# Kernel optimization log

Measured on AMD Instinct MI355X. Metric: run time of the kernel, lower is better.

## Reference

```python
import jax, jax.numpy as jnp
import numpy as np

B, T, H = 16, 512, 512

def _gru_layer(x, h0, wih, whh, bih, bhh, reverse):
    # x: [B,T,in], h0: [B,H]; PyTorch gate order r,z,n in the 3H axis.
    xg = jnp.einsum('bti,gi->btg', x, wih) + bih  # [B,T,3H] input-side gates, precomputed
    def step(h, xg_t):
        gh = h @ whh.T + bhh  # [B,3H]
        xr, xz, xn = jnp.split(xg_t, 3, axis=-1)
        hr, hz, hn = jnp.split(gh, 3, axis=-1)
        r = jax.nn.sigmoid(xr + hr)
        z = jax.nn.sigmoid(xz + hz)
        n = jnp.tanh(xn + r * hn)
        h_new = (1.0 - z) * n + z * h
        return h_new, h_new
    _, ys = jax.lax.scan(step, h0, jnp.swapaxes(xg, 0, 1), reverse=reverse)  # [T,B,H]
    return jnp.swapaxes(ys, 0, 1)

def _forward(x, h1, h2,
             wih_l0f, whh_l0f, bih_l0f, bhh_l0f, wih_l0b, whh_l0b, bih_l0b, bhh_l0b,
             wih_l1f, whh_l1f, bih_l1f, bhh_l1f, wih_l1b, whh_l1b, bih_l1b, bhh_l1b,
             wih_l2f, whh_l2f, bih_l2f, bhh_l2f, wih_l2b, whh_l2b, bih_l2b, bhh_l2b,
             g2_wih, g2_whh, g2_bih, g2_bhh, fc_w, fc_b):
    layers = [((wih_l0f, whh_l0f, bih_l0f, bhh_l0f), (wih_l0b, whh_l0b, bih_l0b, bhh_l0b)),
              ((wih_l1f, whh_l1f, bih_l1f, bhh_l1f), (wih_l1b, whh_l1b, bih_l1b, bhh_l1b)),
              ((wih_l2f, whh_l2f, bih_l2f, bhh_l2f), (wih_l2b, whh_l2b, bih_l2b, bhh_l2b))]
    out = x
    for l, (pf, pb) in enumerate(layers):
        of = _gru_layer(out, h1[2 * l], *pf, reverse=False)
        ob = _gru_layer(out, h1[2 * l + 1], *pb, reverse=True)
        out = jnp.concatenate([of, ob], axis=-1)  # [B,T,2H]
    out2 = _gru_layer(out, h2[0], g2_wih, g2_whh, g2_bih, g2_bhh, reverse=False)  # [B,T,H]
    logits = out2[:, -1, :] @ fc_w.T + fc_b  # [B,1]
    return (jax.nn.sigmoid(logits), out2)

def setup_inputs():
    key = jax.random.key(0)
    ks = jax.random.split(key, 40)
    cnt = iter(range(40))
    s = jnp.float32(0.04)
    d = {}
    d['x'] = jax.random.normal(ks[next(cnt)], (B, T, 2048), jnp.float32)
    d['h1'] = jax.random.normal(ks[next(cnt)], (6, B, H), jnp.float32) * s
    d['h2'] = jax.random.normal(ks[next(cnt)], (1, B, H), jnp.float32) * s
    in_dims = [2048, 2 * H, 2 * H]
    for l in range(3):
        for dr in 'fb':
            d[f'wih_l{l}{dr}'] = jax.random.normal(ks[next(cnt)], (3 * H, in_dims[l]), jnp.float32) * s
            d[f'whh_l{l}{dr}'] = jax.random.normal(ks[next(cnt)], (3 * H, H), jnp.float32) * s
            d[f'bih_l{l}{dr}'] = jax.random.normal(ks[next(cnt)], (3 * H,), jnp.float32) * s
            d[f'bhh_l{l}{dr}'] = jax.random.normal(ks[next(cnt)], (3 * H,), jnp.float32) * s
    d['g2_wih'] = jax.random.normal(ks[next(cnt)], (3 * H, 2 * H), jnp.float32) * s
    d['g2_whh'] = jax.random.normal(ks[next(cnt)], (3 * H, H), jnp.float32) * s
    d['g2_bih'] = jax.random.normal(ks[next(cnt)], (3 * H,), jnp.float32) * s
    d['g2_bhh'] = jax.random.normal(ks[next(cnt)], (3 * H,), jnp.float32) * s
    d['fc_w'] = jax.random.normal(ks[next(cnt)], (1, H), jnp.float32) * s
    d['fc_b'] = jax.random.normal(ks[next(cnt)], (1,), jnp.float32) * s
    return d

def reference(x, h1, h2,
              wih_l0f, whh_l0f, bih_l0f, bhh_l0f, wih_l0b, whh_l0b, bih_l0b, bhh_l0b,
              wih_l1f, whh_l1f, bih_l1f, bhh_l1f, wih_l1b, whh_l1b, bih_l1b, bhh_l1b,
              wih_l2f, whh_l2f, bih_l2f, bhh_l2f, wih_l2b, whh_l2b, bih_l2b, bhh_l2b,
              g2_wih, g2_whh, g2_bih, g2_bhh, fc_w, fc_b):
    return _forward(x, h1, h2,
                    wih_l0f, whh_l0f, bih_l0f, bhh_l0f, wih_l0b, whh_l0b, bih_l0b, bhh_l0b,
                    wih_l1f, whh_l1f, bih_l1f, bhh_l1f, wih_l1b, whh_l1b, bih_l1b, bhh_l1b,
                    wih_l2f, whh_l2f, bih_l2f, bhh_l2f, wih_l2b, whh_l2b, bih_l2b, bhh_l2b,
                    g2_wih, g2_whh, g2_bih, g2_bhh, fc_w, fc_b)
```

## Files before the change

### kernel.cpp

```cpp
#include <hip/hip_runtime.h>
#include <cstdint>
#include <cstddef>

typedef unsigned short u16;
typedef unsigned int u32;
typedef __attribute__((ext_vector_type(8))) short bf16x8;
typedef __attribute__((ext_vector_type(4))) float f32x4;

#define T_SEQ 512
#define HID 512

__device__ __forceinline__ u16 f2bf(float f) {
  union { float f; u32 i; } c; c.f = f;
  u32 r = (c.i + 0x7FFFu + ((c.i >> 16) & 1u)) >> 16;
  return (u16)r;
}
__device__ __forceinline__ u16 f2h(float f) {
  union { _Float16 h; u16 u; } c; c.h = (_Float16)f; return c.u;
}
__device__ __forceinline__ float h2f(u16 u) {
  union { u16 u; _Float16 h; } c; c.u = u; return (float)c.h;
}
__device__ __forceinline__ float sigmf(float x) { return 1.f / (1.f + __expf(-x)); }
__device__ __forceinline__ float tanhfast(float x) {
  float e = __expf(2.f * x); return 1.f - 2.f / (e + 1.f);
}

template <int AF32>
__launch_bounds__(256)
__global__ void gemm_xg(const void* __restrict__ Av,
                        const float* __restrict__ W0, const float* __restrict__ W1,
                        const float* __restrict__ b0, const float* __restrict__ b1,
                        u16* __restrict__ xg0, u16* __restrict__ xg1, int K) {
  const int dir = blockIdx.z;
  const float* W = dir ? W1 : W0;
  const float* bias = dir ? b1 : b0;
  u16* xg = dir ? xg1 : xg0;
  const int bm = blockIdx.x, bn = blockIdx.y;
  const int tid = threadIdx.x, lane = tid & 63, wv = tid >> 6;
  const int wm = wv & 1, wn = wv >> 1, quad = lane >> 4, l15 = lane & 15;

  __shared__ u16 As[128 * 40];
  __shared__ u16 Bs[128 * 40];

  f32x4 acc[4][4] = {};
  const float* Wb = W + (size_t)(bn * 128) * K;

  for (int k0 = 0; k0 < K; k0 += 32) {
    __syncthreads();
    if constexpr (AF32) {
      const float* Ab = (const float*)Av + (size_t)(bm * 128) * K;
#pragma unroll
      for (int it = 0; it < 4; ++it) {
        int c = tid + it * 256;
        int row = c >> 3, kp = (c & 7) * 4;
        float4 v = *(const float4*)(Ab + (size_t)row * K + k0 + kp);
        ushort4 s = { f2bf(v.x), f2bf(v.y), f2bf(v.z), f2bf(v.w) };
        *(ushort4*)(&As[row * 40 + kp]) = s;
      }
    } else {
      const u16* Ab = (const u16*)Av + (size_t)(bm * 128) * K;
#pragma unroll
      for (int it = 0; it < 2; ++it) {
        int c = tid + it * 256;
        int row = c >> 2, kp = (c & 3) * 8;
        *(bf16x8*)(&As[row * 40 + kp]) = *(const bf16x8*)(Ab + (size_t)row * K + k0 + kp);
      }
    }
#pragma unroll
    for (int it = 0; it < 4; ++it) {
      int c = tid + it * 256;
      int row = c >> 3, kp = (c & 7) * 4;
      float4 v = *(const float4*)(Wb + (size_t)row * K + k0 + kp);
      ushort4 s = { f2bf(v.x), f2bf(v.y), f2bf(v.z), f2bf(v.w) };
      *(ushort4*)(&Bs[row * 40 + kp]) = s;
    }
    __syncthreads();
    bf16x8 af[4], bf[4];
#pragma unroll
    for (int i = 0; i < 4; ++i) {
      af[i] = *(const bf16x8*)(&As[(wm * 64 + i * 16 + l15) * 40 + quad * 8]);
      bf[i] = *(const bf16x8*)(&Bs[(wn * 64 + i * 16 + l15) * 40 + quad * 8]);
    }
#pragma unroll
    for (int mi = 0; mi < 4; ++mi)
#pragma unroll
      for (int ni = 0; ni < 4; ++ni)
        acc[mi][ni] = __builtin_amdgcn_mfma_f32_16x16x32_bf16(af[mi], bf[ni], acc[mi][ni], 0, 0, 0);
  }

#pragma unroll
  for (int ni = 0; ni < 4; ++ni) {
    int n = bn * 128 + wn * 64 + ni * 16 + l15;
    float bv = bias[n];
#pragma unroll
    for (int mi = 0; mi < 4; ++mi) {
      int m0 = bm * 128 + wm * 64 + mi * 16 + quad * 4;
#pragma unroll
      for (int r = 0; r < 4; ++r)
        xg[(size_t)(m0 + r) * 1536 + n] = f2h(acc[mi][ni][r] + bv);
    }
  }
}

__launch_bounds__(384, 1)
__global__ void gru_rec(const u16* __restrict__ xg_f, const u16* __restrict__ xg_b,
                        const float* __restrict__ whh_f, const float* __restrict__ whh_b,
                        const float* __restrict__ bhh_f, const float* __restrict__ bhh_b,
                        const float* __restrict__ h0_f, const float* __restrict__ h0_b,
                        void* __restrict__ outp, int out_stride, int out_f32,
                        u16* __restrict__ hbuf, int* __restrict__ counters, int Tn) {
  const int dir = blockIdx.y;
  const u16* xg   = dir ? xg_b  : xg_f;
  const float* whh = dir ? whh_b : whh_f;
  const float* bhh = dir ? bhh_b : bhh_f;
  const float* h0  = dir ? h0_b  : h0_f;
  const int w = blockIdx.x;
  const int tid = threadIdx.x, lane = tid & 63, wv = tid >> 6;
  const int quad = lane >> 4, l15 = lane & 15;
  int* cnt = counters + dir * 1024;
  u16* hb0 = hbuf + (dir * 2 + 0) * (16 * 512);
  u16* hb1 = hbuf + (dir * 2 + 1) * (16 * 512);
  const int dir_off = dir * 512;

  __shared__ float glds[3][16][64];
  __shared__ float hprev[16][64];
  __shared__ u16 xlds[3][16][64];
  __shared__ float bhl[3][64];

  bf16x8 bfr[2][16];
#pragma unroll
  for (int f = 0; f < 2; ++f) {
    int fl = wv * 2 + f;
    int g = fl >> 2, q = fl & 3;
    int row = g * 512 + (w * 4 + q) * 16 + l15;
    const float* wp = whh + (size_t)row * 512 + quad * 8;
#pragma unroll
    for (int kt = 0; kt < 16; ++kt) {
      float4 a = *(const float4*)(wp + kt * 32);
      float4 b = *(const float4*)(wp + kt * 32 + 4);
      bf16x8 fr;
      fr[0] = (short)f2bf(a.x); fr[1] = (short)f2bf(a.y);
      fr[2] = (short)f2bf(a.z); fr[3] = (short)f2bf(a.w);
      fr[4] = (short)f2bf(b.x); fr[5] = (short)f2bf(b.y);
      fr[6] = (short)f2bf(b.z); fr[7] = (short)f2bf(b.w);
      bfr[f][kt] = fr;
    }
  }
  for (int i = tid; i < 512; i += 384) {
    int b = i >> 5, j2 = (i & 31) * 2;
    float v0 = h0[b * 512 + w * 64 + j2];
    float v1 = h0[b * 512 + w * 64 + j2 + 1];
    hprev[b][j2] = v0; hprev[b][j2 + 1] = v1;
    u32 pk = (u32)f2bf(v0) | ((u32)f2bf(v1) << 16);
    __hip_atomic_store((u32*)(hb1 + b * 512 + w * 64 + j2), pk,
                       __ATOMIC_RELAXED, __HIP_MEMORY_SCOPE_AGENT);
  }
  for (int i = tid; i < 192; i += 384) {
    int g = i >> 6, jl = i & 63;
    bhl[g][jl] = bhh[g * 512 + w * 64 + jl];
  }
  __syncthreads();
  if (tid == 0)
    __hip_atomic_fetch_add(&cnt[0], 1, __ATOMIC_RELEASE, __HIP_MEMORY_SCOPE_AGENT);

  for (int t = 0; t < Tn; ++t) {
    const int te = dir ? (Tn - 1 - t) : t;
    for (int i = tid; i < 768; i += 384) {
      int g = i >> 8, r2 = i & 255, b = r2 >> 4, j4 = (r2 & 15) * 4;
      uint2 v = *(const uint2*)(xg + ((size_t)(b * Tn + te)) * 1536 + g * 512 + w * 64 + j4);
      *(uint2*)(&xlds[g][b][j4]) = v;
    }
    if (tid == 0) {
      while (__hip_atomic_load(&cnt[t], __ATOMIC_RELAXED, __HIP_MEMORY_SCOPE_AGENT) < 8)
        __builtin_amdgcn_s_sleep(1);
      (void)__hip_atomic_load(&cnt[t], __ATOMIC_ACQUIRE, __HIP_MEMORY_SCOPE_AGENT);
    }
    __syncthreads();

    const u16* hsrc = (t & 1) ? hb0 : hb1;
    const u16* hp = hsrc + l15 * 512 + quad * 8;
    bf16x8 afr[16];
#pragma unroll
    for (int kt = 0; kt < 16; ++kt) afr[kt] = *(const bf16x8*)(hp + kt * 32);

#pragma unroll
    for (int f = 0; f < 2; ++f) {
      f32x4 acc = {0.f, 0.f, 0.f, 0.f};
#pragma unroll
      for (int kt = 0; kt < 16; ++kt)
        acc = __builtin_amdgcn_mfma_f32_16x16x32_bf16(afr[kt], bfr[f][kt], acc, 0, 0, 0);
      int fl = wv * 2 + f, g = fl >> 2, q = fl & 3;
#pragma unroll
      for (int r = 0; r < 4; ++r) glds[g][quad * 4 + r][q * 16 + l15] = acc[r];
    }
    __syncthreads();

    u16* hbw = (t & 1) ? hb1 : hb0;
    for (int i = tid; i < 512; i += 384) {
      int b = i >> 5, j2 = (i & 31) * 2;
      float hn2[2];
#pragma unroll
      for (int u = 0; u < 2; ++u) {
        int jl = j2 + u;
        float xr = h2f(xlds[0][b][jl]);
        float xz = h2f(xlds[1][b][jl]);
        float xn = h2f(xlds[2][b][jl]);
        float hr = glds[0][b][jl] + bhl[0][jl];
        float hz = glds[1][b][jl] + bhl[1][jl];
        float hnn = glds[2][b][jl] + bhl[2][jl];
        float r = sigmf(xr + hr);
        float z = sigmf(xz + hz);
        float n = tanhfast(xn + r * hnn);
        float hv = (1.f - z) * n + z * hprev[b][jl];
        hprev[b][jl] = hv;
        hn2[u] = hv;
      }
      u32 pk = (u32)f2bf(hn2[0]) | ((u32)f2bf(hn2[1]) << 16);
      __hip_atomic_store((u32*)(hbw + b * 512 + w * 64 + j2), pk,
                         __ATOMIC_RELAXED, __HIP_MEMORY_SCOPE_AGENT);
      if (out_f32) {
        float2 o = { hn2[0], hn2[1] };
        *(float2*)((float*)outp + (size_t)(b * Tn + te) * out_stride + dir_off + w * 64 + j2) = o;
      } else {
        *(u32*)((u16*)outp + (size_t)(b * Tn + te) * out_stride + dir_off + w * 64 + j2) = pk;
      }
    }
    __syncthreads();
    if (tid == 0)
      __hip_atomic_fetch_add(&cnt[t + 1], 1, __ATOMIC_RELEASE, __HIP_MEMORY_SCOPE_AGENT);
  }
}

__global__ void fc_kernel(const float* __restrict__ out2, const float* __restrict__ fc_w,
                          const float* __restrict__ fc_b, float* __restrict__ dst) {
  int b = blockIdx.x, lane = threadIdx.x;
  const float* row = out2 + ((size_t)b * T_SEQ + (T_SEQ - 1)) * HID;
  float s = 0.f;
  for (int j = lane; j < HID; j += 64) s += row[j] * fc_w[j];
#pragma unroll
  for (int off = 32; off > 0; off >>= 1) s += __shfl_down(s, off, 64);
  if (lane == 0) dst[b] = sigmf(s + fc_b[0]);
}

extern "C" void kernel_launch(void* const* d_in, const int* in_sizes, int n_in,
                              void* d_out, int out_size, void* d_ws, size_t ws_size,
                              hipStream_t stream) {
  const float* x  = (const float*)d_in[0];
  const float* h1 = (const float*)d_in[1];
  const float* h2 = (const float*)d_in[2];
  auto P = [&](int i) { return (const float*)d_in[i]; };

  u16* xg0 = (u16*)d_ws;
  u16* xg1 = xg0 + (size_t)8192 * 1536;
  u16* outb = xg1 + (size_t)8192 * 1536;
  u16* hbuf = outb + (size_t)8192 * 1024;
  int* counters = (int*)(hbuf + 4 * 8192);
  float* out_f = (float*)d_out;
  float* out2 = out_f + 16;

  hipMemsetAsync(counters, 0, 8192 * sizeof(int), stream);

  gemm_xg<1><<<dim3(64, 12, 2), 256, 0, stream>>>(x, P(3), P(7), P(5), P(9), xg0, xg1, 2048);
  gru_rec<<<dim3(8, 2), 384, 0, stream>>>(xg0, xg1, P(4), P(8), P(6), P(10),
                                          h1, h1 + 8192, outb, 1024, 0, hbuf, counters, T_SEQ);
  gemm_xg<0><<<dim3(64, 12, 2), 256, 0, stream>>>(outb, P(11), P(15), P(13), P(17), xg0, xg1, 1024);
  gru_rec<<<dim3(8, 2), 384, 0, stream>>>(xg0, xg1, P(12), P(16), P(14), P(18),
                                          h1 + 2 * 8192, h1 + 3 * 8192, outb, 1024, 0, hbuf,
                                          counters + 2048, T_SEQ);
  gemm_xg<0><<<dim3(64, 12, 2), 256, 0, stream>>>(outb, P(19), P(23), P(21), P(25), xg0, xg1, 1024);
  gru_rec<<<dim3(8, 2), 384, 0, stream>>>(xg0, xg1, P(20), P(24), P(22), P(26),
                                          h1 + 4 * 8192, h1 + 5 * 8192, outb, 1024, 0, hbuf,
                                          counters + 4096, T_SEQ);
  gemm_xg<0><<<dim3(64, 12, 1), 256, 0, stream>>>(outb, P(27), P(27), P(29), P(29), xg0, xg1, 1024);
  gru_rec<<<dim3(8, 1), 384, 0, stream>>>(xg0, xg0, P(28), P(28), P(30), P(30),
                                          h2, h2, out2, 512, 1, hbuf, counters + 6144, T_SEQ);
  fc_kernel<<<16, 64, 0, stream>>>(out2, P(31), P(32), out_f);
}
```

Baseline: 11.90 ms.

## Use per-wave flags and register-resident gates to remove block barriers in GRU recurrence

Reworks the recurrent kernel so each wave owns 16 hidden units across all three gates, keeping the MFMA accumulators, hidden state and biases in registers instead of staging them through LDS. The per-timestep block counter and its __syncthreads barriers are replaced with per-wave monotonic flags, polled wave-wide with __any, so waves synchronise directly with their producers. The aim is to shorten the serial critical path of every timestep. In exchange there are 32 flags to poll, more register pressure from 48 weight fragments per wave, and scattered 2-byte xg loads per step.

```diff
diff --git a/kernel.cpp b/kernel.cpp
--- a/kernel.cpp
+++ b/kernel.cpp
@@ -103,38 +103,32 @@
   }
 }
 
-__launch_bounds__(384, 1)
+__launch_bounds__(256, 1)
 __global__ void gru_rec(const u16* __restrict__ xg_f, const u16* __restrict__ xg_b,
                         const float* __restrict__ whh_f, const float* __restrict__ whh_b,
                         const float* __restrict__ bhh_f, const float* __restrict__ bhh_b,
                         const float* __restrict__ h0_f, const float* __restrict__ h0_b,
                         void* __restrict__ outp, int out_stride, int out_f32,
-                        u16* __restrict__ hbuf, int* __restrict__ counters, int Tn) {
+                        u16* __restrict__ hbuf, int* __restrict__ flags_base, int Tn) {
   const int dir = blockIdx.y;
-  const u16* xg   = dir ? xg_b  : xg_f;
+  const u16* xg    = dir ? xg_b  : xg_f;
   const float* whh = dir ? whh_b : whh_f;
   const float* bhh = dir ? bhh_b : bhh_f;
   const float* h0  = dir ? h0_b  : h0_f;
   const int w = blockIdx.x;
-  const int tid = threadIdx.x, lane = tid & 63, wv = tid >> 6;
+  const int tid = threadIdx.x, lane = tid & 63, q = tid >> 6;
   const int quad = lane >> 4, l15 = lane & 15;
-  int* cnt = counters + dir * 1024;
+  const int j = w * 64 + q * 16 + l15;
+  const int myflag = w * 4 + q;
+  int* flags = flags_base + dir * 64;
   u16* hb0 = hbuf + (dir * 2 + 0) * (16 * 512);
   u16* hb1 = hbuf + (dir * 2 + 1) * (16 * 512);
   const int dir_off = dir * 512;
 
-  __shared__ float glds[3][16][64];
-  __shared__ float hprev[16][64];
-  __shared__ u16 xlds[3][16][64];
-  __shared__ float bhl[3][64];
-
-  bf16x8 bfr[2][16];
-#pragma unroll
-  for (int f = 0; f < 2; ++f) {
-    int fl = wv * 2 + f;
-    int g = fl >> 2, q = fl & 3;
-    int row = g * 512 + (w * 4 + q) * 16 + l15;
-    const float* wp = whh + (size_t)row * 512 + quad * 8;
+  bf16x8 wfr[3][16];
+#pragma unroll
+  for (int g = 0; g < 3; ++g) {
+    const float* wp = whh + (size_t)(g * 512 + j) * 512 + quad * 8;
 #pragma unroll
     for (int kt = 0; kt < 16; ++kt) {
       float4 a = *(const float4*)(wp + kt * 32);
@@ -144,39 +138,47 @@
       fr[2] = (short)f2bf(a.z); fr[3] = (short)f2bf(a.w);
       fr[4] = (short)f2bf(b.x); fr[5] = (short)f2bf(b.y);
       fr[6] = (short)f2bf(b.z); fr[7] = (short)f2bf(b.w);
-      bfr[f][kt] = fr;
-    }
-  }
-  for (int i = tid; i < 512; i += 384) {
-    int b = i >> 5, j2 = (i & 31) * 2;
-    float v0 = h0[b * 512 + w * 64 + j2];
-    float v1 = h0[b * 512 + w * 64 + j2 + 1];
-    hprev[b][j2] = v0; hprev[b][j2 + 1] = v1;
-    u32 pk = (u32)f2bf(v0) | ((u32)f2bf(v1) << 16);
-    __hip_atomic_store((u32*)(hb1 + b * 512 + w * 64 + j2), pk,
-                       __ATOMIC_RELAXED, __HIP_MEMORY_SCOPE_AGENT);
-  }
-  for (int i = tid; i < 192; i += 384) {
-    int g = i >> 6, jl = i & 63;
-    bhl[g][jl] = bhh[g * 512 + w * 64 + jl];
-  }
-  __syncthreads();
-  if (tid == 0)
-    __hip_atomic_fetch_add(&cnt[0], 1, __ATOMIC_RELEASE, __HIP_MEMORY_SCOPE_AGENT);
+      wfr[g][kt] = fr;
+    }
+  }
+  float bh[3];
+#pragma unroll
+  for (int g = 0; g < 3; ++g) bh[g] = bhh[g * 512 + j];
+
+  float hp4[4];
+  u32 sv[4];
+#pragma unroll
+  for (int r = 0; r < 4; ++r) {
+    int b = quad * 4 + r;
+    hp4[r] = h0[b * 512 + j];
+    u32 m = f2bf(hp4[r]);
+    u32 nb = (u32)__shfl_xor((int)m, 1);
+    sv[r] = m | (nb << 16);
+  }
+  if (!(l15 & 1)) {
+#pragma unroll
+    for (int r = 0; r < 4; ++r)
+      __hip_atomic_store((u32*)(hb1 + (quad * 4 + r) * 512 + j), sv[r],
+                         __ATOMIC_RELAXED, __HIP_MEMORY_SCOPE_AGENT);
+  }
+  if (lane == 0)
+    __hip_atomic_store(&flags[myflag], 1, __ATOMIC_RELEASE, __HIP_MEMORY_SCOPE_AGENT);
 
   for (int t = 0; t < Tn; ++t) {
     const int te = dir ? (Tn - 1 - t) : t;
-    for (int i = tid; i < 768; i += 384) {
-      int g = i >> 8, r2 = i & 255, b = r2 >> 4, j4 = (r2 & 15) * 4;
-      uint2 v = *(const uint2*)(xg + ((size_t)(b * Tn + te)) * 1536 + g * 512 + w * 64 + j4);
-      *(uint2*)(&xlds[g][b][j4]) = v;
-    }
-    if (tid == 0) {
-      while (__hip_atomic_load(&cnt[t], __ATOMIC_RELAXED, __HIP_MEMORY_SCOPE_AGENT) < 8)
-        __builtin_amdgcn_s_sleep(1);
-      (void)__hip_atomic_load(&cnt[t], __ATOMIC_ACQUIRE, __HIP_MEMORY_SCOPE_AGENT);
-    }
-    __syncthreads();
+    u16 xgv[3][4];
+#pragma unroll
+    for (int g = 0; g < 3; ++g)
+#pragma unroll
+      for (int r = 0; r < 4; ++r)
+        xgv[g][r] = xg[(size_t)((quad * 4 + r) * Tn + te) * 1536 + g * 512 + j];
+
+    const int need = t + 1;
+    int fv = __hip_atomic_load(&flags[lane & 31], __ATOMIC_ACQUIRE, __HIP_MEMORY_SCOPE_AGENT);
+    while (__any(fv < need)) {
+      __builtin_amdgcn_s_sleep(1);
+      fv = __hip_atomic_load(&flags[lane & 31], __ATOMIC_ACQUIRE, __HIP_MEMORY_SCOPE_AGENT);
+    }
 
     const u16* hsrc = (t & 1) ? hb0 : hb1;
     const u16* hp = hsrc + l15 * 512 + quad * 8;
@@ -184,51 +186,48 @@
 #pragma unroll
     for (int kt = 0; kt < 16; ++kt) afr[kt] = *(const bf16x8*)(hp + kt * 32);
 
-#pragma unroll
-    for (int f = 0; f < 2; ++f) {
-      f32x4 acc = {0.f, 0.f, 0.f, 0.f};
-#pragma unroll
-      for (int kt = 0; kt < 16; ++kt)
-        acc = __builtin_amdgcn_mfma_f32_16x16x32_bf16(afr[kt], bfr[f][kt], acc, 0, 0, 0);
-      int fl = wv * 2 + f, g = fl >> 2, q = fl & 3;
-#pragma unroll
-      for (int r = 0; r < 4; ++r) glds[g][quad * 4 + r][q * 16 + l15] = acc[r];
-    }
-    __syncthreads();
+    f32x4 acc[3] = {};
+#pragma unroll
+    for (int kt = 0; kt < 16; ++kt)
+#pragma unroll
+      for (int g = 0; g < 3; ++g)
+        acc[g] = __builtin_amdgcn_mfma_f32_16x16x32_bf16(afr[kt], wfr[g][kt], acc[g], 0, 0, 0);
 
     u16* hbw = (t & 1) ? hb1 : hb0;
-    for (int i = tid; i < 512; i += 384) {
-      int b = i >> 5, j2 = (i & 31) * 2;
-      float hn2[2];
-#pragma unroll
-      for (int u = 0; u < 2; ++u) {
-        int jl = j2 + u;
-        float xr = h2f(xlds[0][b][jl]);
-        float xz = h2f(xlds[1][b][jl]);
-        float xn = h2f(xlds[2][b][jl]);
-        float hr = glds[0][b][jl] + bhl[0][jl];
-        float hz = glds[1][b][jl] + bhl[1][jl];
-        float hnn = glds[2][b][jl] + bhl[2][jl];
-        float r = sigmf(xr + hr);
-        float z = sigmf(xz + hz);
-        float n = tanhfast(xn + r * hnn);
-        float hv = (1.f - z) * n + z * hprev[b][jl];
-        hprev[b][jl] = hv;
-        hn2[u] = hv;
-      }
-      u32 pk = (u32)f2bf(hn2[0]) | ((u32)f2bf(hn2[1]) << 16);
-      __hip_atomic_store((u32*)(hbw + b * 512 + w * 64 + j2), pk,
-                         __ATOMIC_RELAXED, __HIP_MEMORY_SCOPE_AGENT);
-      if (out_f32) {
-        float2 o = { hn2[0], hn2[1] };
-        *(float2*)((float*)outp + (size_t)(b * Tn + te) * out_stride + dir_off + w * 64 + j2) = o;
-      } else {
-        *(u32*)((u16*)outp + (size_t)(b * Tn + te) * out_stride + dir_off + w * 64 + j2) = pk;
-      }
-    }
-    __syncthreads();
-    if (tid == 0)
-      __hip_atomic_fetch_add(&cnt[t + 1], 1, __ATOMIC_RELEASE, __HIP_MEMORY_SCOPE_AGENT);
+    float hv4[4];
+#pragma unroll
+    for (int r = 0; r < 4; ++r) {
+      float xr = h2f(xgv[0][r]);
+      float xz = h2f(xgv[1][r]);
+      float xn = h2f(xgv[2][r]);
+      float rg = sigmf(xr + acc[0][r] + bh[0]);
+      float zg = sigmf(xz + acc[1][r] + bh[1]);
+      float ng = tanhfast(xn + rg * (acc[2][r] + bh[2]));
+      float hv = (1.f - zg) * ng + zg * hp4[r];
+      hp4[r] = hv;
+      hv4[r] = hv;
+      u32 m = f2bf(hv);
+      u32 nb = (u32)__shfl_xor((int)m, 1);
+      sv[r] = m | (nb << 16);
+    }
+    if (!(l15 & 1)) {
+#pragma unroll
+      for (int r = 0; r < 4; ++r)
+        __hip_atomic_store((u32*)(hbw + (quad * 4 + r) * 512 + j), sv[r],
+                           __ATOMIC_RELAXED, __HIP_MEMORY_SCOPE_AGENT);
+    }
+    if (lane == 0)
+      __hip_atomic_store(&flags[myflag], t + 2, __ATOMIC_RELEASE, __HIP_MEMORY_SCOPE_AGENT);
+
+    if (out_f32) {
+#pragma unroll
+      for (int r = 0; r < 4; ++r)
+        ((float*)outp)[(size_t)((quad * 4 + r) * Tn + te) * out_stride + dir_off + j] = hv4[r];
+    } else if (!(l15 & 1)) {
+#pragma unroll
+      for (int r = 0; r < 4; ++r)
+        *(u32*)((u16*)outp + (size_t)((quad * 4 + r) * Tn + te) * out_stride + dir_off + j) = sv[r];
+    }
   }
 }
 
@@ -237,7 +236,7 @@
   int b = blockIdx.x, lane = threadIdx.x;
   const float* row = out2 + ((size_t)b * T_SEQ + (T_SEQ - 1)) * HID;
   float s = 0.f;
-  for (int j = lane; j < HID; j += 64) s += row[j] * fc_w[j];
+  for (int jj = lane; jj < HID; jj += 64) s += row[jj] * fc_w[jj];
 #pragma unroll
   for (int off = 32; off > 0; off >>= 1) s += __shfl_down(s, off, 64);
   if (lane == 0) dst[b] = sigmf(s + fc_b[0]);
@@ -255,25 +254,25 @@
   u16* xg1 = xg0 + (size_t)8192 * 1536;
   u16* outb = xg1 + (size_t)8192 * 1536;
   u16* hbuf = outb + (size_t)8192 * 1024;
-  int* counters = (int*)(hbuf + 4 * 8192);
+  int* flags = (int*)(hbuf + 4 * 8192);
   float* out_f = (float*)d_out;
   float* out2 = out_f + 16;
 
-  hipMemsetAsync(counters, 0, 8192 * sizeof(int), stream);
+  hipMemsetAsync(flags, 0, 4 * 128 * sizeof(int), stream);
 
   gemm_xg<1><<<dim3(64, 12, 2), 256, 0, stream>>>(x, P(3), P(7), P(5), P(9), xg0, xg1, 2048);
-  gru_rec<<<dim3(8, 2), 384, 0, stream>>>(xg0, xg1, P(4), P(8), P(6), P(10),
-                                          h1, h1 + 8192, outb, 1024, 0, hbuf, counters, T_SEQ);
+  gru_rec<<<dim3(8, 2), 256, 0, stream>>>(xg0, xg1, P(4), P(8), P(6), P(10),
+                                          h1, h1 + 8192, outb, 1024, 0, hbuf, flags, T_SEQ);
   gemm_xg<0><<<dim3(64, 12, 2), 256, 0, stream>>>(outb, P(11), P(15), P(13), P(17), xg0, xg1, 1024);
-  gru_rec<<<dim3(8, 2), 384, 0, stream>>>(xg0, xg1, P(12), P(16), P(14), P(18),
+  gru_rec<<<dim3(8, 2), 256, 0, stream>>>(xg0, xg1, P(12), P(16), P(14), P(18),
                                           h1 + 2 * 8192, h1 + 3 * 8192, outb, 1024, 0, hbuf,
-                                          counters + 2048, T_SEQ);
+                                          flags + 128, T_SEQ);
   gemm_xg<0><<<dim3(64, 12, 2), 256, 0, stream>>>(outb, P(19), P(23), P(21), P(25), xg0, xg1, 1024);
-  gru_rec<<<dim3(8, 2), 384, 0, stream>>>(xg0, xg1, P(20), P(24), P(22), P(26),
+  gru_rec<<<dim3(8, 2), 256, 0, stream>>>(xg0, xg1, P(20), P(24), P(22), P(26),
                                           h1 + 4 * 8192, h1 + 5 * 8192, outb, 1024, 0, hbuf,
-                                          counters + 4096, T_SEQ);
+                                          flags + 256, T_SEQ);
   gemm_xg<0><<<dim3(64, 12, 1), 256, 0, stream>>>(outb, P(27), P(27), P(29), P(29), xg0, xg1, 1024);
-  gru_rec<<<dim3(8, 1), 384, 0, stream>>>(xg0, xg0, P(28), P(28), P(30), P(30),
-                                          h2, h2, out2, 512, 1, hbuf, counters + 6144, T_SEQ);
+  gru_rec<<<dim3(8, 1), 256, 0, stream>>>(xg0, xg0, P(28), P(28), P(30), P(30),
+                                          h2, h2, out2, 512, 1, hbuf, flags + 384, T_SEQ);
   fc_kernel<<<16, 64, 0, stream>>>(out2, P(31), P(32), out_f);
 }
```

Result: slower. 14.55 ms (+22.2%).
